# Optimization experiments

Hardware: AMD Instinct MI355X
Metric: run time of the kernel (lower is better)

## Reference

```python
import jax, jax.numpy as jnp
import numpy as np


def setup_inputs() -> dict:
    key = jax.random.key(0)
    k1, k2, k3 = jax.random.split(key, 3)
    B, T1, T2, D = 16, 1024, 1024, 256
    x = jax.random.normal(k1, (B, T1, D), dtype=jnp.float32)
    y = jax.random.normal(k2, (B, T2, D), dtype=jnp.float32)
    WS = jax.random.normal(k3, (3 * D,), dtype=jnp.float32) * 0.05
    return {"x": x, "y": y, "WS": WS}


def reference(x, y, WS):
    # BiDAF trilinear similarity. Original computes
    #   S[b,i,j] = sum_k concat([x_i, 1, x_i])_k * concat([1, y_j, y_j])_k * WS_k
    # which decomposes exactly into:
    #   S = x @ w1 (broadcast over j) + y @ w2 (broadcast over i) + (x * w3) @ y^T
    D = x.shape[-1]
    w1, w2, w3 = WS[:D], WS[D:2 * D], WS[2 * D:]
    term_x = jnp.einsum('bid,d->bi', x, w1)            # [B, T1]
    term_y = jnp.einsum('bjd,d->bj', y, w2)            # [B, T2]
    term_xy = jnp.einsum('bid,bjd->bij', x * w3, y)    # [B, T1, T2]
    return term_xy + term_x[:, :, None] + term_y[:, None, :]
```

## Files before the change

kernel.cpp:

```cpp
#include <hip/hip_runtime.h>

#define DK 256
#define TT 1024
#define NB 16

typedef __attribute__((ext_vector_type(8))) short bf16x8;
typedef __attribute__((ext_vector_type(4))) float f32x4;

__device__ __forceinline__ unsigned short f2bf(float f) {
    unsigned int u = __float_as_uint(f);
    unsigned int r = 0x7fffu + ((u >> 16) & 1u);
    return (unsigned short)((u + r) >> 16);
}

__global__ __launch_bounds__(256) void prep_kernel(
    const float* __restrict__ x, const float* __restrict__ y,
    const float* __restrict__ WS,
    unsigned short* __restrict__ xw, unsigned short* __restrict__ yb,
    float* __restrict__ tx, float* __restrict__ ty)
{
    const int wid  = threadIdx.x >> 6;
    const int lane = threadIdx.x & 63;
    const int row  = blockIdx.x * 4 + wid;
    const bool is_x = row < NB * TT;
    const int r = is_x ? row : row - NB * TT;

    const float4 wmul = is_x ? ((const float4*)(WS + 2 * DK))[lane]
                             : make_float4(1.f, 1.f, 1.f, 1.f);
    const float4 wdot = is_x ? ((const float4*)WS)[lane]
                             : ((const float4*)(WS + DK))[lane];

    const float4 v = ((const float4*)((is_x ? x : y) + (size_t)r * DK))[lane];

    float partial = v.x * wdot.x + v.y * wdot.y + v.z * wdot.z + v.w * wdot.w;

    ushort4 o;
    o.x = f2bf(v.x * wmul.x);
    o.y = f2bf(v.y * wmul.y);
    o.z = f2bf(v.z * wmul.z);
    o.w = f2bf(v.w * wmul.w);
    ((ushort4*)((is_x ? xw : yb) + (size_t)r * DK))[lane] = o;

    #pragma unroll
    for (int off = 32; off > 0; off >>= 1)
        partial += __shfl_down(partial, off);
    if (lane == 0) (is_x ? tx : ty)[r] = partial;
}

__device__ __forceinline__ void gl_lds16(const unsigned short* g,
                                         unsigned short* l)
{
    __builtin_amdgcn_global_load_lds(
        (const __attribute__((address_space(1))) void*)g,
        (__attribute__((address_space(3))) void*)l,
        16, 0, 0);
}

__global__ __launch_bounds__(256, 2) void gemm_kernel(
    const unsigned short* __restrict__ xw, const unsigned short* __restrict__ yb,
    const float* __restrict__ tx, const float* __restrict__ ty,
    float* __restrict__ out)
{
    __shared__ unsigned short Bs[128 * DK];

    const int tid  = threadIdx.x;
    const int w    = tid >> 6;
    const int lane = tid & 63;
    const int jt = blockIdx.x;
    const int is = blockIdx.y;
    const int b  = blockIdx.z;

    const unsigned short* gB = yb + ((size_t)b * TT + jt * 128) * DK;

    #pragma unroll
    for (int q = 0; q < 16; ++q) {
        const int g = w * 16 + q;
        const int j = g * 2 + (lane >> 5);
        const int s = lane & 31;
        const int c = s ^ (j & 7);
        gl_lds16(gB + j * DK + c * 8, Bs + g * 512);
    }
    __syncthreads();

    const int mfr  = lane & 15;
    const int quad = lane >> 4;
    const int i0   = is * 256 + w * 64;
    const unsigned short* gA = xw + ((size_t)b * TT + i0) * DK;

    f32x4 acc[4][8];
    #pragma unroll
    for (int it = 0; it < 4; ++it)
        #pragma unroll
        for (int n = 0; n < 8; ++n)
            acc[it][n] = (f32x4){0.f, 0.f, 0.f, 0.f};

    #pragma unroll
    for (int ks = 0; ks < 8; ++ks) {
        bf16x8 av[4];
        #pragma unroll
        for (int it = 0; it < 4; ++it)
            av[it] = *(const bf16x8*)(gA + (size_t)(it * 16 + mfr) * DK
                                      + ks * 32 + quad * 8);
        #pragma unroll
        for (int n = 0; n < 8; ++n) {
            const int j    = n * 16 + mfr;
            const int slot = (ks * 4 + quad) ^ (j & 7);
            const bf16x8 bv = *(const bf16x8*)(Bs + j * DK + slot * 8);
            #pragma unroll
            for (int it = 0; it < 4; ++it)
                acc[it][n] = __builtin_amdgcn_mfma_f32_16x16x32_bf16(
                    av[it], bv, acc[it][n], 0, 0, 0);
        }
    }

    const float* txp = tx + b * TT + i0;
    const float* typ = ty + b * TT + jt * 128;
    float tyv[8];
    #pragma unroll
    for (int n = 0; n < 8; ++n)
        tyv[n] = typ[n * 16 + mfr];

    float* outB = out + ((size_t)b << 20) + (size_t)i0 * TT + jt * 128;
    #pragma unroll
    for (int it = 0; it < 4; ++it) {
        #pragma unroll
        for (int r = 0; r < 4; ++r) {
            const int row  = it * 16 + quad * 4 + r;
            const float trow = txp[row];
            #pragma unroll
            for (int n = 0; n < 8; ++n)
                outB[(size_t)row * TT + n * 16 + mfr] = acc[it][n][r] + trow + tyv[n];
        }
    }
}

__global__ __launch_bounds__(256) void naive_kernel(
    const float* __restrict__ x, const float* __restrict__ y,
    const float* __restrict__ WS, float* __restrict__ out)
{
    size_t idx = (size_t)blockIdx.x * 256 + threadIdx.x;
    if (idx >= (size_t)NB * TT * TT) return;
    const int b = (int)(idx >> 20);
    const int i = (int)((idx >> 10) & (TT - 1));
    const int j = (int)(idx & (TT - 1));
    const float* xp = x + ((size_t)b * TT + i) * DK;
    const float* yp = y + ((size_t)b * TT + j) * DK;
    float s = 0.f, sx = 0.f, sy = 0.f;
    for (int d = 0; d < DK; ++d) {
        const float xv = xp[d], yv = yp[d];
        s  += xv * WS[2 * DK + d] * yv;
        sx += xv * WS[d];
        sy += yv * WS[DK + d];
    }
    out[idx] = s + sx + sy;
}

extern "C" void kernel_launch(void* const* d_in, const int* in_sizes, int n_in,
                              void* d_out, int out_size, void* d_ws, size_t ws_size,
                              hipStream_t stream)
{
    const float* x  = (const float*)d_in[0];
    const float* y  = (const float*)d_in[1];
    const float* WS = (const float*)d_in[2];
    float* out = (float*)d_out;

    const size_t n_xy = (size_t)NB * TT * DK;
    const size_t need = n_xy * 2 * sizeof(unsigned short)
                      + (size_t)NB * TT * 2 * sizeof(float);

    if (ws_size >= need) {
        unsigned short* xw = (unsigned short*)d_ws;
        unsigned short* yb = xw + n_xy;
        float* tx = (float*)(yb + n_xy);
        float* ty = tx + NB * TT;

        prep_kernel<<<dim3((2 * NB * TT) / 4), dim3(256), 0, stream>>>(
            x, y, WS, xw, yb, tx, ty);
        gemm_kernel<<<dim3(8, 4, NB), dim3(256), 0, stream>>>(
            xw, yb, tx, ty, out);
    } else {
        naive_kernel<<<dim3((NB * TT * TT + 255) / 256), dim3(256), 0, stream>>>(
            x, y, WS, out);
    }
}
```

Before: 111.0 us.

## Fuse bf16 conversion and linear terms into single GEMM kernel

Removes the separate prep kernel and its bf16 workspace, converting y (scaled by w3) to bf16 directly into LDS and converting x to bf16 in registers inside the GEMM loop. The x and y linear terms are computed on the fly, using shuffle reductions for x and LDS for y. This saves one launch and the workspace write and read round trip. In exchange each block rereads fp32 inputs (twice the bytes of bf16), x is reread by all 8 column blocks, and the conversion ALU work is repeated per tile.

```diff
diff --git a/kernel.cpp b/kernel.cpp
--- a/kernel.cpp
+++ b/kernel.cpp
@@ -5,6 +5,7 @@
 #define NB 16
 
 typedef __attribute__((ext_vector_type(8))) short bf16x8;
+typedef __attribute__((ext_vector_type(8))) unsigned short u16x8;
 typedef __attribute__((ext_vector_type(4))) float f32x4;
 
 __device__ __forceinline__ unsigned short f2bf(float f) {
@@ -13,79 +14,57 @@
     return (unsigned short)((u + r) >> 16);
 }
 
-__global__ __launch_bounds__(256) void prep_kernel(
+__global__ __launch_bounds__(256, 2) void fused_kernel(
     const float* __restrict__ x, const float* __restrict__ y,
-    const float* __restrict__ WS,
-    unsigned short* __restrict__ xw, unsigned short* __restrict__ yb,
-    float* __restrict__ tx, float* __restrict__ ty)
-{
-    const int wid  = threadIdx.x >> 6;
-    const int lane = threadIdx.x & 63;
-    const int row  = blockIdx.x * 4 + wid;
-    const bool is_x = row < NB * TT;
-    const int r = is_x ? row : row - NB * TT;
-
-    const float4 wmul = is_x ? ((const float4*)(WS + 2 * DK))[lane]
-                             : make_float4(1.f, 1.f, 1.f, 1.f);
-    const float4 wdot = is_x ? ((const float4*)WS)[lane]
-                             : ((const float4*)(WS + DK))[lane];
-
-    const float4 v = ((const float4*)((is_x ? x : y) + (size_t)r * DK))[lane];
-
-    float partial = v.x * wdot.x + v.y * wdot.y + v.z * wdot.z + v.w * wdot.w;
-
-    ushort4 o;
-    o.x = f2bf(v.x * wmul.x);
-    o.y = f2bf(v.y * wmul.y);
-    o.z = f2bf(v.z * wmul.z);
-    o.w = f2bf(v.w * wmul.w);
-    ((ushort4*)((is_x ? xw : yb) + (size_t)r * DK))[lane] = o;
-
-    #pragma unroll
-    for (int off = 32; off > 0; off >>= 1)
-        partial += __shfl_down(partial, off);
-    if (lane == 0) (is_x ? tx : ty)[r] = partial;
-}
-
-__device__ __forceinline__ void gl_lds16(const unsigned short* g,
-                                         unsigned short* l)
-{
-    __builtin_amdgcn_global_load_lds(
-        (const __attribute__((address_space(1))) void*)g,
-        (__attribute__((address_space(3))) void*)l,
-        16, 0, 0);
-}
-
-__global__ __launch_bounds__(256, 2) void gemm_kernel(
-    const unsigned short* __restrict__ xw, const unsigned short* __restrict__ yb,
-    const float* __restrict__ tx, const float* __restrict__ ty,
-    float* __restrict__ out)
+    const float* __restrict__ WS, float* __restrict__ out)
 {
     __shared__ unsigned short Bs[128 * DK];
+    __shared__ float tys[128];
 
     const int tid  = threadIdx.x;
+    const int lane = tid & 63;
     const int w    = tid >> 6;
-    const int lane = tid & 63;
     const int jt = blockIdx.x;
     const int is = blockIdx.y;
     const int b  = blockIdx.z;
 
-    const unsigned short* gB = yb + ((size_t)b * TT + jt * 128) * DK;
-
-    #pragma unroll
-    for (int q = 0; q < 16; ++q) {
-        const int g = w * 16 + q;
-        const int j = g * 2 + (lane >> 5);
-        const int s = lane & 31;
-        const int c = s ^ (j & 7);
-        gl_lds16(gB + j * DK + c * 8, Bs + g * 512);
+    {
+        const int j = tid >> 1;
+        const int h = tid & 1;
+        const float* gY  = y + ((size_t)b * TT + jt * 128 + j) * DK + h * 128;
+        const float* w3p = WS + 2 * DK + h * 128;
+        const float* w2p = WS + DK + h * 128;
+        unsigned short* Brow = Bs + j * DK;
+        float typ = 0.f;
+        #pragma unroll
+        for (int c = 0; c < 16; ++c) {
+            const int d0 = c * 8;
+            const float4 ya = *(const float4*)(gY + d0);
+            const float4 yb = *(const float4*)(gY + d0 + 4);
+            const float4 wa = *(const float4*)(w3p + d0);
+            const float4 wb = *(const float4*)(w3p + d0 + 4);
+            const float4 va = *(const float4*)(w2p + d0);
+            const float4 vb = *(const float4*)(w2p + d0 + 4);
+            typ += ya.x * va.x + ya.y * va.y + ya.z * va.z + ya.w * va.w
+                 + yb.x * vb.x + yb.y * vb.y + yb.z * vb.z + yb.w * vb.w;
+            u16x8 o;
+            o[0] = f2bf(ya.x * wa.x); o[1] = f2bf(ya.y * wa.y);
+            o[2] = f2bf(ya.z * wa.z); o[3] = f2bf(ya.w * wa.w);
+            o[4] = f2bf(yb.x * wb.x); o[5] = f2bf(yb.y * wb.y);
+            o[6] = f2bf(yb.z * wb.z); o[7] = f2bf(yb.w * wb.w);
+            const int cg   = h * 16 + c;
+            const int slot = cg ^ (j & 7);
+            *(u16x8*)(Brow + slot * 8) = o;
+        }
+        typ += __shfl_xor(typ, 1);
+        if (h == 0) tys[j] = typ;
     }
     __syncthreads();
 
     const int mfr  = lane & 15;
     const int quad = lane >> 4;
     const int i0   = is * 256 + w * 64;
-    const unsigned short* gA = xw + ((size_t)b * TT + i0) * DK;
+    const float* gA = x + ((size_t)b * TT + i0) * DK;
 
     f32x4 acc[4][8];
     #pragma unroll
@@ -93,14 +72,29 @@
         #pragma unroll
         for (int n = 0; n < 8; ++n)
             acc[it][n] = (f32x4){0.f, 0.f, 0.f, 0.f};
+    float txp[4] = {0.f, 0.f, 0.f, 0.f};
 
     #pragma unroll
     for (int ks = 0; ks < 8; ++ks) {
+        const float* w1p = WS + ks * 32 + quad * 8;
+        const float4 w1a = *(const float4*)(w1p);
+        const float4 w1b = *(const float4*)(w1p + 4);
         bf16x8 av[4];
         #pragma unroll
-        for (int it = 0; it < 4; ++it)
-            av[it] = *(const bf16x8*)(gA + (size_t)(it * 16 + mfr) * DK
-                                      + ks * 32 + quad * 8);
+        for (int it = 0; it < 4; ++it) {
+            const float* rp = gA + (size_t)(it * 16 + mfr) * DK
+                              + ks * 32 + quad * 8;
+            const float4 xa = *(const float4*)rp;
+            const float4 xb = *(const float4*)(rp + 4);
+            txp[it] += xa.x * w1a.x + xa.y * w1a.y + xa.z * w1a.z + xa.w * w1a.w
+                     + xb.x * w1b.x + xb.y * w1b.y + xb.z * w1b.z + xb.w * w1b.w;
+            bf16x8 a;
+            a[0] = (short)f2bf(xa.x); a[1] = (short)f2bf(xa.y);
+            a[2] = (short)f2bf(xa.z); a[3] = (short)f2bf(xa.w);
+            a[4] = (short)f2bf(xb.x); a[5] = (short)f2bf(xb.y);
+            a[6] = (short)f2bf(xb.z); a[7] = (short)f2bf(xb.w);
+            av[it] = a;
+        }
         #pragma unroll
         for (int n = 0; n < 8; ++n) {
             const int j    = n * 16 + mfr;
@@ -113,46 +107,30 @@
         }
     }
 
-    const float* txp = tx + b * TT + i0;
-    const float* typ = ty + b * TT + jt * 128;
+    #pragma unroll
+    for (int it = 0; it < 4; ++it) {
+        txp[it] += __shfl_xor(txp[it], 16);
+        txp[it] += __shfl_xor(txp[it], 32);
+    }
+
     float tyv[8];
     #pragma unroll
     for (int n = 0; n < 8; ++n)
-        tyv[n] = typ[n * 16 + mfr];
+        tyv[n] = tys[n * 16 + mfr];
 
     float* outB = out + ((size_t)b << 20) + (size_t)i0 * TT + jt * 128;
     #pragma unroll
     for (int it = 0; it < 4; ++it) {
         #pragma unroll
         for (int r = 0; r < 4; ++r) {
-            const int row  = it * 16 + quad * 4 + r;
-            const float trow = txp[row];
+            const int row = it * 16 + quad * 4 + r;
+            const float trow = __shfl(txp[it], (lane & 48) | (quad * 4 + r));
             #pragma unroll
             for (int n = 0; n < 8; ++n)
-                outB[(size_t)row * TT + n * 16 + mfr] = acc[it][n][r] + trow + tyv[n];
+                outB[(size_t)row * TT + n * 16 + mfr] =
+                    acc[it][n][r] + trow + tyv[n];
         }
     }
-}
-
-__global__ __launch_bounds__(256) void naive_kernel(
-    const float* __restrict__ x, const float* __restrict__ y,
-    const float* __restrict__ WS, float* __restrict__ out)
-{
-    size_t idx = (size_t)blockIdx.x * 256 + threadIdx.x;
-    if (idx >= (size_t)NB * TT * TT) return;
-    const int b = (int)(idx >> 20);
-    const int i = (int)((idx >> 10) & (TT - 1));
-    const int j = (int)(idx & (TT - 1));
-    const float* xp = x + ((size_t)b * TT + i) * DK;
-    const float* yp = y + ((size_t)b * TT + j) * DK;
-    float s = 0.f, sx = 0.f, sy = 0.f;
-    for (int d = 0; d < DK; ++d) {
-        const float xv = xp[d], yv = yp[d];
-        s  += xv * WS[2 * DK + d] * yv;
-        sx += xv * WS[d];
-        sy += yv * WS[DK + d];
-    }
-    out[idx] = s + sx + sy;
 }
 
 extern "C" void kernel_launch(void* const* d_in, const int* in_sizes, int n_in,
@@ -163,23 +141,7 @@
     const float* y  = (const float*)d_in[1];
     const float* WS = (const float*)d_in[2];
     float* out = (float*)d_out;
+    (void)d_ws; (void)ws_size;
 
-    const size_t n_xy = (size_t)NB * TT * DK;
-    const size_t need = n_xy * 2 * sizeof(unsigned short)
-                      + (size_t)NB * TT * 2 * sizeof(float);
-
-    if (ws_size >= need) {
-        unsigned short* xw = (unsigned short*)d_ws;
-        unsigned short* yb = xw + n_xy;
-        float* tx = (float*)(yb + n_xy);
-        float* ty = tx + NB * TT;
-
-        prep_kernel<<<dim3((2 * NB * TT) / 4), dim3(256), 0, stream>>>(
-            x, y, WS, xw, yb, tx, ty);
-        gemm_kernel<<<dim3(8, 4, NB), dim3(256), 0, stream>>>(
-            xw, yb, tx, ty, out);
-    } else {
-        naive_kernel<<<dim3((NB * TT * TT + 255) / 256), dim3(256), 0, stream>>>(
-            x, y, WS, out);
-    }
+    fused_kernel<<<dim3(8, 4, NB), dim3(256), 0, stream>>>(x, y, WS, out);
 }
```

Result: slower. 122.3 us (+10.1%).
